# Kernel optimization log

Hardware: AMD Instinct MI355X
Metric: run time of the kernel (lower is better)

Reference implementation:

```python
import jax, jax.numpy as jnp
import numpy as np

B, S, D_IN = 128, 196, 512
H, DK, RATIO = 8, 32, 4
DV = RATIO * DK                      # 128
QKV_DIM = H * (2 * DK + DV)          # 1536
PROJ_IN = H * DV                     # 1024
EPS = 1e-3                           # keras BatchNormalization default epsilon
SCALE = DK ** (-0.5)


def hard_swish(x):
    return x * jnp.clip(x + 3.0, 0.0, 6.0) * (1.0 / 6.0)


def setup_inputs() -> dict:
    key = jax.random.key(0)
    ks = jax.random.split(key, 12)
    inp = {
        "x": jax.random.normal(ks[0], (B, S, D_IN), dtype=jnp.float32),
        "W_qkv": jax.random.normal(ks[1], (D_IN, QKV_DIM), dtype=jnp.float32) * (D_IN ** -0.5),
        "b_qkv": jnp.zeros((QKV_DIM,), dtype=jnp.float32),
        "gamma1": jnp.ones((QKV_DIM,), dtype=jnp.float32),
        "beta1": jnp.zeros((QKV_DIM,), dtype=jnp.float32),
        "mean1": jax.random.normal(ks[2], (QKV_DIM,), dtype=jnp.float32) * 0.1,
        "var1": jax.random.uniform(ks[3], (QKV_DIM,), minval=0.5, maxval=1.5, dtype=jnp.float32),
        "W_proj": jax.random.normal(ks[4], (PROJ_IN, D_IN), dtype=jnp.float32) * (PROJ_IN ** -0.5),
        "b_proj": jnp.zeros((D_IN,), dtype=jnp.float32),
        "gamma2": jnp.ones((D_IN,), dtype=jnp.float32),
        "beta2": jnp.zeros((D_IN,), dtype=jnp.float32),
        "mean2": jax.random.normal(ks[5], (D_IN,), dtype=jnp.float32) * 0.1,
        "var2": jax.random.uniform(ks[6], (D_IN,), minval=0.5, maxval=1.5, dtype=jnp.float32),
    }
    return inp


def _bn(x, gamma, beta, mean, var):
    # inference-mode BatchNorm over the last (channel) axis
    return (x - mean) * jax.lax.rsqrt(var + EPS) * gamma + beta


def reference(x, W_qkv, b_qkv, gamma1, beta1, mean1, var1,
              W_proj, b_proj, gamma2, beta2, mean2, var2):
    # QKV projection + BN
    qkv = _bn(x @ W_qkv + b_qkv, gamma1, beta1, mean1, var1)      # [B,S,1536]
    qkv = qkv.reshape(B, S, H, 2 * DK + DV)
    q, k, v = jnp.split(qkv, [DK, 2 * DK], axis=3)                # [B,S,H,*]
    q = jnp.transpose(q, (0, 2, 1, 3))                            # [B,H,S,DK]
    k = jnp.transpose(k, (0, 2, 1, 3))
    v = jnp.transpose(v, (0, 2, 1, 3))                            # [B,H,S,DV]
    attn = jax.nn.softmax(jnp.einsum("bhqd,bhkd->bhqk", q, k) * SCALE, axis=-1)
    av = jnp.einsum("bhqk,bhkd->bhqd", attn, v)                   # [B,H,S,DV]
    # faithful to original: transpose to [B,H,DV,S] then reshape to [B,S,H*DV]
    hidden = jnp.transpose(av, (0, 1, 3, 2)).reshape(B, S, PROJ_IN)
    hidden = hard_swish(hidden)
    out = _bn(hidden @ W_proj + b_proj, gamma2, beta2, mean2, var2)  # [B,S,512]
    return out
```

## Files before the change

### kernel.cpp

```cpp
#include <hip/hip_runtime.h>
#include <math.h>

namespace {

constexpr int Bb   = 128;
constexpr int Ss   = 196;
constexpr int DIN  = 512;
constexpr int Hh   = 8;
constexpr int DKc  = 32;
constexpr int DVc  = 128;
constexpr int QKVD = 1536;
constexpr int PIN  = 1024;
constexpr int Mrows = Bb * Ss;
constexpr float EPSc   = 1e-3f;
constexpr float SCALEc = 0.17677669529663687f;

typedef __bf16 bf16x8 __attribute__((ext_vector_type(8)));
typedef __bf16 bf16x4 __attribute__((ext_vector_type(4)));
typedef float  f32x4  __attribute__((ext_vector_type(4)));

constexpr int VT_STRIDE = 232;
constexpr size_t VT_QELEMS = 8192;
constexpr size_t VT_BH = 4 * VT_QELEMS;

__device__ __forceinline__ void gl_lds16(const void* g, void* l) {
    __builtin_amdgcn_global_load_lds(
        (const __attribute__((address_space(1))) void*)g,
        (__attribute__((address_space(3))) void*)l, 16, 0, 0);
}

__global__ __launch_bounds__(256)
void prep(const float* __restrict__ W1, __bf16* __restrict__ WT1o,
          const float* __restrict__ W2, __bf16* __restrict__ WT2o,
          const float* __restrict__ x, __bf16* __restrict__ xb)
{
    int id = blockIdx.x;
    if (id >= 1280) {
        const int i = (id - 1280) * 256 + threadIdx.x;
        float4 v = ((const float4*)x)[i];
        bf16x4 o = { (__bf16)v.x, (__bf16)v.y, (__bf16)v.z, (__bf16)v.w };
        ((bf16x4*)xb)[i] = o;
        return;
    }
    __shared__ float tile[32][33];
    const float* W; __bf16* WT; int K, N, bx, by;
    if (id < 768) { W = W1; WT = WT1o; K = 512;  N = 1536; bx = id % 48; by = id / 48; }
    else { id -= 768; W = W2; WT = WT2o; K = 1024; N = 512;  bx = id % 16; by = id / 16; }
    const int n0 = bx * 32, k0 = by * 32;
    const int tx = threadIdx.x & 31, ty = threadIdx.x >> 5;
#pragma unroll
    for (int i = ty; i < 32; i += 8)
        tile[i][tx] = W[(size_t)(k0 + i) * N + n0 + tx];
    __syncthreads();
#pragma unroll
    for (int i = ty; i < 32; i += 8)
        WT[(size_t)(n0 + i) * K + k0 + tx] = (__bf16)tile[tx][i];
}

__global__ __launch_bounds__(256)
void gemm1_bn_scatter(const __bf16* __restrict__ A, const __bf16* __restrict__ BT,
                      const float* __restrict__ bias, const float* __restrict__ gamma,
                      const float* __restrict__ beta, const float* __restrict__ mean,
                      const float* __restrict__ var,
                      __bf16* __restrict__ qkvO, __bf16* __restrict__ VTp)
{
    constexpr int N = QKVD, K = DIN;
    constexpr int BM = 128, BN = 128;
    __shared__ __align__(16) char sm[65536];

    const int t    = threadIdx.x;
    const int wave = t >> 6;
    const int lane = t & 63;
    const int lr   = lane & 15;
    const int q    = lane >> 4;

    constexpr int ntiles = N / BN;
    constexpr int nwg = 196 * ntiles;
    const int bid = (blockIdx.x & 7) * (nwg >> 3) + (blockIdx.x >> 3);
    const int m0 = (bid / ntiles) * BM;
    const int n0 = (bid % ntiles) * BN;
    const int wm = (wave & 1) * 64;
    const int wn = (wave >> 1) * 64;

    const __bf16* aG0 = A  + (size_t)(m0 + (t >> 2)) * K + (t & 3) * 8;
    const __bf16* aG1 = aG0 + (size_t)64 * K;
    const __bf16* bG0 = BT + (size_t)(n0 + (t >> 2)) * K + (t & 3) * 8;
    const __bf16* bG1 = bG0 + (size_t)64 * K;

    auto STAGE = [&](int k0, int cur) {
        char* lA = sm + cur * 16384 + wave * 1024;
        char* lB = sm + 32768 + cur * 16384 + wave * 1024;
        gl_lds16(aG0 + k0,      lA);
        gl_lds16(aG1 + k0,      lA + 4096);
        gl_lds16(aG0 + k0 + 32, lA + 8192);
        gl_lds16(aG1 + k0 + 32, lA + 8192 + 4096);
        gl_lds16(bG0 + k0,      lB);
        gl_lds16(bG1 + k0,      lB + 4096);
        gl_lds16(bG0 + k0 + 32, lB + 8192);
        gl_lds16(bG1 + k0 + 32, lB + 8192 + 4096);
    };

    f32x4 acc[4][4] = {};

    STAGE(0, 0);
    __syncthreads();
    int cur = 0;
    for (int k0 = 0; k0 < K; k0 += 64) {
        if (k0 + 64 < K) STAGE(k0 + 64, cur ^ 1);
        const __bf16* Abuf = (const __bf16*)(sm + cur * 16384);
        const __bf16* Bbuf = (const __bf16*)(sm + 32768 + cur * 16384);
#pragma unroll
        for (int kk = 0; kk < 2; ++kk) {
            bf16x8 aF[4], bF[4];
#pragma unroll
            for (int i = 0; i < 4; ++i)
                aF[i] = *(const bf16x8*)(Abuf + kk * 4096 + (wm + i * 16 + lr) * 32 + q * 8);
#pragma unroll
            for (int j = 0; j < 4; ++j)
                bF[j] = *(const bf16x8*)(Bbuf + kk * 4096 + (wn + j * 16 + lr) * 32 + q * 8);
#pragma unroll
            for (int i = 0; i < 4; ++i)
#pragma unroll
                for (int j = 0; j < 4; ++j)
                    acc[i][j] = __builtin_amdgcn_mfma_f32_16x16x32_bf16(
                        aF[i], bF[j], acc[i][j], 0, 0, 0);
        }
        __syncthreads();
        cur ^= 1;
    }

    const int tmod = n0 % 384;
    const int cq0  = (tmod == 0) ? 0 : (tmod == 128 ? 64 : -1);
    const int vc0  = (tmod == 0) ? 64 : 0;
    const int nv   = (tmod == 256) ? 128 : 64;
    const bool qk_wave = (tmod == 0) ? (wn == 0) : (tmod == 128 ? (wn == 64) : false);

    __bf16* qkreg = (__bf16*)sm;
    __bf16* vreg  = (__bf16*)(sm + ((nv == 128) ? 0 : 18432));
    const int vbase = (nv == 128) ? wn : 0;

#pragma unroll
    for (int j = 0; j < 4; ++j) {
        const int n = n0 + wn + j * 16 + lr;
        const float s  = gamma[n] * rsqrtf(var[n] + EPSc);
        const float tv = fmaf(bias[n] - mean[n], s, beta[n]);
        if (qk_wave) {
#pragma unroll
            for (int i = 0; i < 4; ++i) {
                const int row = wm + i * 16 + q * 4;
#pragma unroll
                for (int r = 0; r < 4; ++r)
                    qkreg[(row + r) * 72 + j * 16 + lr] = (__bf16)fmaf(acc[i][j][r], s, tv);
            }
        } else {
#pragma unroll
            for (int i = 0; i < 4; ++i) {
                bf16x4 pk = { (__bf16)fmaf(acc[i][j][0], s, tv),
                              (__bf16)fmaf(acc[i][j][1], s, tv),
                              (__bf16)fmaf(acc[i][j][2], s, tv),
                              (__bf16)fmaf(acc[i][j][3], s, tv) };
                *(bf16x4*)(vreg + (vbase + j * 16 + lr) * 136 + wm + i * 16 + q * 4) = pk;
            }
        }
    }
    __syncthreads();

    if (cq0 >= 0) {
#pragma unroll
        for (int rr = 0; rr < 4; ++rr) {
            const int row = rr * 32 + (t >> 3);
            const int l   = t & 7;
            bf16x8 vv = *(const bf16x8*)(qkreg + row * 72 + l * 8);
            *(bf16x8*)(qkvO + (size_t)(m0 + row) * N + n0 + cq0 + l * 8) = vv;
        }
    }
    const int iters = (nv * 16) / 256;
    for (int it = 0; it < iters; ++it) {
        const int a  = it * 256 + t;
        const int cl = a >> 4;
        const int r0 = (a & 15) * 8;
        const int n  = n0 + vc0 + cl;
        const int h  = n / 192;
        const int d  = n - h * 192 - 64;
        const int mr = m0 + r0;
        const int b_ = mr / 196;
        const int s0 = mr - b_ * 196;
        __bf16* dst0 = VTp + (size_t)(b_ * 8 + h) * VT_BH
                     + (size_t)(d >> 5) * VT_QELEMS + (size_t)(d & 31) * VT_STRIDE;
        bf16x8 vv = *(const bf16x8*)(vreg + cl * 136 + r0);
        if (s0 <= 188) {
            *(bf16x8*)(dst0 + s0) = vv;
        } else {
#pragma unroll
            for (int e = 0; e < 8; ++e) {
                int se = s0 + e;
                __bf16* dst = dst0;
                if (se >= 196) { se -= 196; dst += 8 * VT_BH; }
                dst[se] = vv[e];
            }
        }
    }
}

template<int N, int K>
__global__ __launch_bounds__(256)
void gemm_bn_mfma(const __bf16* __restrict__ A, const __bf16* __restrict__ BT,
                  const float* __restrict__ bias, const float* __restrict__ gamma,
                  const float* __restrict__ beta, const float* __restrict__ mean,
                  const float* __restrict__ var, float* __restrict__ C)
{
    constexpr int BM = 128, BN = 128;
    __shared__ __align__(16) char sm[65536];
    const int t    = threadIdx.x;
    const int wave = t >> 6;
    const int lane = t & 63;
    const int lr   = lane & 15;
    const int q    = lane >> 4;
    constexpr int ntiles = N / BN;
    constexpr int nwg = 196 * ntiles;
    const int bid = (blockIdx.x & 7) * (nwg >> 3) + (blockIdx.x >> 3);
    const int m0 = (bid / ntiles) * BM;
    const int n0 = (bid % ntiles) * BN;
    const int wm = (wave & 1) * 64;
    const int wn = (wave >> 1) * 64;
    const __bf16* aG0 = A  + (size_t)(m0 + (t >> 2)) * K + (t & 3) * 8;
    const __bf16* aG1 = aG0 + (size_t)64 * K;
    const __bf16* bG0 = BT + (size_t)(n0 + (t >> 2)) * K + (t & 3) * 8;
    const __bf16* bG1 = bG0 + (size_t)64 * K;

    auto STAGE = [&](int k0, int cur) {
        char* lA = sm + cur * 16384 + wave * 1024;
        char* lB = sm + 32768 + cur * 16384 + wave * 1024;
        gl_lds16(aG0 + k0,      lA);
        gl_lds16(aG1 + k0,      lA + 4096);
        gl_lds16(aG0 + k0 + 32, lA + 8192);
        gl_lds16(aG1 + k0 + 32, lA + 8192 + 4096);
        gl_lds16(bG0 + k0,      lB);
        gl_lds16(bG1 + k0,      lB + 4096);
        gl_lds16(bG0 + k0 + 32, lB + 8192);
        gl_lds16(bG1 + k0 + 32, lB + 8192 + 4096);
    };

    f32x4 acc[4][4] = {};

    STAGE(0, 0);
    __syncthreads();
    int cur = 0;
    for (int k0 = 0; k0 < K; k0 += 64) {
        if (k0 + 64 < K) STAGE(k0 + 64, cur ^ 1);
        const __bf16* Abuf = (const __bf16*)(sm + cur * 16384);
        const __bf16* Bbuf = (const __bf16*)(sm + 32768 + cur * 16384);
#pragma unroll
        for (int kk = 0; kk < 2; ++kk) {
            bf16x8 aF[4], bF[4];
#pragma unroll
            for (int i = 0; i < 4; ++i)
                aF[i] = *(const bf16x8*)(Abuf + kk * 4096 + (wm + i * 16 + lr) * 32 + q * 8);
#pragma unroll
            for (int j = 0; j < 4; ++j)
                bF[j] = *(const bf16x8*)(Bbuf + kk * 4096 + (wn + j * 16 + lr) * 32 + q * 8);
#pragma unroll
            for (int i = 0; i < 4; ++i)
#pragma unroll
                for (int j = 0; j < 4; ++j)
                    acc[i][j] = __builtin_amdgcn_mfma_f32_16x16x32_bf16(
                        aF[i], bF[j], acc[i][j], 0, 0, 0);
        }
        __syncthreads();
        cur ^= 1;
    }
#pragma unroll
    for (int j = 0; j < 4; ++j) {
        const int n = n0 + wn + j * 16 + lr;
        const float s  = gamma[n] * rsqrtf(var[n] + EPSc);
        const float tv = fmaf(bias[n] - mean[n], s, beta[n]);
#pragma unroll
        for (int i = 0; i < 4; ++i) {
            const int mrow = m0 + wm + i * 16 + q * 4;
#pragma unroll
            for (int r = 0; r < 4; ++r)
                C[(size_t)(mrow + r) * N + n] = fmaf(acc[i][j][r], s, tv);
        }
    }
}

__global__ __launch_bounds__(1024)
void attn_mfma(const __bf16* __restrict__ qkv, const __bf16* __restrict__ VTp,
               __bf16* __restrict__ hidden)
{
    __shared__ __align__(16) char smem[145920];
    __bf16* Kb = (__bf16*)smem;

    const int t = threadIdx.x;
    const int wave = t >> 6, lane = t & 63;
    const int lr = lane & 15, q = lane >> 4;
    const int bh = blockIdx.x;
    const int b = bh >> 3, h = bh & 7;
    const __bf16* qkvb = qkv + (size_t)b * 196 * QKVD + h * 192;

    const char* gV = (const char*)(VTp + (size_t)bh * VT_BH);
    char* ldsV = smem + 113152;
    gl_lds16(gV + wave * 1024 + lane * 16, ldsV + wave * 1024);

    if (t < 196 * 4) {
        const int s = t >> 2, c = t & 3;
        bf16x8 v = *(const bf16x8*)(qkvb + (size_t)s * QKVD + 32 + c * 8);
        *(bf16x8*)(Kb + s * 40 + c * 8) = v;
    }

    __syncthreads();

    const int qt = wave;
    const bool wactive = (qt <= 12);
    __bf16* Pw = (__bf16*)(smem + 16640 + (wactive ? qt : 0) * 7424);

    if (wactive) {
        int sQ = qt * 16 + lr; if (sQ > 195) sQ = 195;
        bf16x8 aQ = *(const bf16x8*)(qkv + ((size_t)b * 196 + sQ) * QKVD + h * 192 + q * 8);

        f32x4 sc[13];
#pragma unroll
        for (int nt = 0; nt < 13; ++nt) {
            bf16x8 bK = *(const bf16x8*)(Kb + (nt * 16 + lr) * 40 + q * 8);
            f32x4 z = {0.f, 0.f, 0.f, 0.f};
            sc[nt] = __builtin_amdgcn_mfma_f32_16x16x32_bf16(aQ, bK, z, 0, 0, 0);
        }
        float mrow[4] = {-1e30f, -1e30f, -1e30f, -1e30f};
#pragma unroll
        for (int nt = 0; nt < 13; ++nt) {
            const bool valid = (nt < 12) | (lr < 4);
#pragma unroll
            for (int r = 0; r < 4; ++r) {
                float x = sc[nt][r] * SCALEc;
                sc[nt][r] = x;
                if (valid) mrow[r] = fmaxf(mrow[r], x);
            }
        }
#pragma unroll
        for (int d = 1; d < 16; d <<= 1)
#pragma unroll
            for (int r = 0; r < 4; ++r)
                mrow[r] = fmaxf(mrow[r], __shfl_xor(mrow[r], d, 64));
        float l[4] = {0.f, 0.f, 0.f, 0.f};
#pragma unroll
        for (int nt = 0; nt < 13; ++nt) {
            const bool valid = (nt < 12) | (lr < 4);
#pragma unroll
            for (int r = 0; r < 4; ++r) {
                float e = valid ? __expf(sc[nt][r] - mrow[r]) : 0.f;
                sc[nt][r] = e;
                l[r] += e;
            }
        }
#pragma unroll
        for (int d = 1; d < 16; d <<= 1)
#pragma unroll
            for (int r = 0; r < 4; ++r)
                l[r] += __shfl_xor(l[r], d, 64);
        float inv[4];
#pragma unroll
        for (int r = 0; r < 4; ++r) inv[r] = 1.f / l[r];

#pragma unroll
        for (int nt = 0; nt < 13; ++nt)
#pragma unroll
            for (int r = 0; r < 4; ++r)
                Pw[(q * 4 + r) * 232 + nt * 16 + lr] = (__bf16)(sc[nt][r] * inv[r]);
        for (int idx = lane; idx < 16 * 24; idx += 64) {
            int row = idx & 15, cz = 208 + (idx >> 4);
            Pw[row * 232 + cz] = (__bf16)0.f;
        }
    }

    const int sbase = qt * 16 + q * 4;
    const bool sval = wactive && (sbase + 3 < 196);
    __bf16* hb = hidden + (size_t)b * 200704 + (size_t)h * 25088;

    for (int q4 = 0; q4 < 4; ++q4) {
        const __bf16* Vl = (const __bf16*)(ldsV + (q4 & 1) * 16384);
        if (q4 < 3)
            gl_lds16(gV + (size_t)(q4 + 1) * 16384 + wave * 1024 + lane * 16,
                     ldsV + ((q4 + 1) & 1) * 16384 + wave * 1024);
        if (wactive) {
            f32x4 o0 = {0.f, 0.f, 0.f, 0.f}, o1 = {0.f, 0.f, 0.f, 0.f};
#pragma unroll
            for (int kk = 0; kk < 7; ++kk) {
                bf16x8 aP = *(const bf16x8*)(Pw + lr * 232 + kk * 32 + q * 8);
                bf16x8 b0 = *(const bf16x8*)(Vl + lr * 232 + kk * 32 + q * 8);
                bf16x8 b1 = *(const bf16x8*)(Vl + (16 + lr) * 232 + kk * 32 + q * 8);
                o0 = __builtin_amdgcn_mfma_f32_16x16x32_bf16(aP, b0, o0, 0, 0, 0);
                o1 = __builtin_amdgcn_mfma_f32_16x16x32_bf16(aP, b1, o1, 0, 0, 0);
            }
            if (sval) {
#pragma unroll
                for (int nt2 = 0; nt2 < 2; ++nt2) {
                    f32x4 o = nt2 ? o1 : o0;
                    const int d = q4 * 32 + nt2 * 16 + lr;
                    bf16x4 pk;
#pragma unroll
                    for (int r = 0; r < 4; ++r) {
                        float x = o[r];
                        pk[r] = (__bf16)(x * fminf(fmaxf(x + 3.f, 0.f), 6.f) * (1.f / 6.f));
                    }
                    *(bf16x4*)(hb + (size_t)d * 196 + sbase) = pk;
                }
            }
        }
        if (q4 < 3) __syncthreads();
    }
}

}

extern "C" void kernel_launch(void* const* d_in, const int* in_sizes, int n_in,
                              void* d_out, int out_size, void* d_ws, size_t ws_size,
                              hipStream_t stream)
{
    const float* x    = (const float*)d_in[0];
    const float* Wqkv = (const float*)d_in[1];
    const float* bqkv = (const float*)d_in[2];
    const float* g1   = (const float*)d_in[3];
    const float* be1  = (const float*)d_in[4];
    const float* mu1  = (const float*)d_in[5];
    const float* va1  = (const float*)d_in[6];
    const float* Wp   = (const float*)d_in[7];
    const float* bp   = (const float*)d_in[8];
    const float* g2   = (const float*)d_in[9];
    const float* be2  = (const float*)d_in[10];
    const float* mu2  = (const float*)d_in[11];
    const float* va2  = (const float*)d_in[12];

    char* ws = (char*)d_ws;
    __bf16* qkv    = (__bf16*)ws;
    __bf16* VTp    = (__bf16*)(ws + 77070336);
    __bf16* hidden = (__bf16*)(ws + 144179200);
    __bf16* xb     = (__bf16*)(ws + 195559424);
    __bf16* WT1    = (__bf16*)(ws + 221249536);
    __bf16* WT2    = (__bf16*)(ws + 222822400);
    float*  out    = (float*)d_out;

    prep<<<dim3(13824), dim3(256), 0, stream>>>(Wqkv, WT1, Wp, WT2, x, xb);

    gemm1_bn_scatter<<<dim3(196 * (QKVD / 128)), dim3(256), 0, stream>>>(
        xb, WT1, bqkv, g1, be1, mu1, va1, qkv, VTp);

    attn_mfma<<<dim3(Bb * Hh), dim3(1024), 0, stream>>>(qkv, VTp, hidden);

    gemm_bn_mfma<DIN, PIN><<<dim3(196 * (DIN / 128)), dim3(256), 0, stream>>>(
        hidden, WT2, bp, g2, be2, mu2, va2, out);
}
```

Baseline: 263.0 us.

## Restructure QKV GEMM with 128x256 tiles, triple-buffered XOR-swizzled LDS pipeline

Rewrites the QKV projection GEMM to use 512-thread workgroups with 128x256 output tiles. K-tiles of 64 are loaded through a three-stage LDS ring with XOR swizzling to avoid bank conflicts, and explicit vmcnt waits let loads overlap the MFMA work. The epilogue becomes per-wave: each wave decides whether its 64-column slice is Q/K or V and stages it in its own LDS region, so no block-wide sync is needed before the stores. In exchange it uses 144KB of LDS per block and manual waitcnt/barrier scheduling, which limits occupancy and is fragile.

```diff
diff --git a/kernel.cpp b/kernel.cpp
--- a/kernel.cpp
+++ b/kernel.cpp
@@ -57,146 +57,165 @@
         WT[(size_t)(n0 + i) * K + k0 + tx] = (__bf16)tile[tx][i];
 }
 
-__global__ __launch_bounds__(256)
+__global__ __launch_bounds__(512)
 void gemm1_bn_scatter(const __bf16* __restrict__ A, const __bf16* __restrict__ BT,
                       const float* __restrict__ bias, const float* __restrict__ gamma,
                       const float* __restrict__ beta, const float* __restrict__ mean,
                       const float* __restrict__ var,
                       __bf16* __restrict__ qkvO, __bf16* __restrict__ VTp)
 {
-    constexpr int N = QKVD, K = DIN;
-    constexpr int BM = 128, BN = 128;
-    __shared__ __align__(16) char sm[65536];
+    constexpr int K = DIN;
+    __shared__ __align__(16) char sm[147456];
 
     const int t    = threadIdx.x;
-    const int wave = t >> 6;
+    const int wid  = t >> 6;
     const int lane = t & 63;
     const int lr   = lane & 15;
     const int q    = lane >> 4;
 
-    constexpr int ntiles = N / BN;
+    constexpr int ntiles = 6;
     constexpr int nwg = 196 * ntiles;
     const int bid = (blockIdx.x & 7) * (nwg >> 3) + (blockIdx.x >> 3);
-    const int m0 = (bid / ntiles) * BM;
-    const int n0 = (bid % ntiles) * BN;
-    const int wm = (wave & 1) * 64;
-    const int wn = (wave >> 1) * 64;
-
-    const __bf16* aG0 = A  + (size_t)(m0 + (t >> 2)) * K + (t & 3) * 8;
-    const __bf16* aG1 = aG0 + (size_t)64 * K;
-    const __bf16* bG0 = BT + (size_t)(n0 + (t >> 2)) * K + (t & 3) * 8;
-    const __bf16* bG1 = bG0 + (size_t)64 * K;
-
-    auto STAGE = [&](int k0, int cur) {
-        char* lA = sm + cur * 16384 + wave * 1024;
-        char* lB = sm + 32768 + cur * 16384 + wave * 1024;
-        gl_lds16(aG0 + k0,      lA);
-        gl_lds16(aG1 + k0,      lA + 4096);
-        gl_lds16(aG0 + k0 + 32, lA + 8192);
-        gl_lds16(aG1 + k0 + 32, lA + 8192 + 4096);
-        gl_lds16(bG0 + k0,      lB);
-        gl_lds16(bG1 + k0,      lB + 4096);
-        gl_lds16(bG0 + k0 + 32, lB + 8192);
-        gl_lds16(bG1 + k0 + 32, lB + 8192 + 4096);
+    const int m0 = (bid / ntiles) * 128;
+    const int n0 = (bid % ntiles) * 256;
+    const int wm  = (wid & 1) * 64;
+    const int wnL = (wid >> 1) * 64;
+
+    char* ring0 = sm;
+    char* ring1 = sm + 49152;
+    char* ring2 = sm + 98304;
+    char* rings[3] = { ring0, ring1, ring2 };
+
+    auto STAGE = [&](int kt, char* rg) {
+#pragma unroll
+        for (int e = 0; e < 2; ++e) {
+            const int c = e * 512 + t;
+            const int gsrc = (c & 7) ^ ((c >> 3) & 7);
+            gl_lds16(A + (size_t)(m0 + (c >> 3)) * K + kt * 64 + gsrc * 8,
+                     rg + c * 16);
+        }
+#pragma unroll
+        for (int e = 0; e < 4; ++e) {
+            const int c = e * 512 + t;
+            const int gsrc = (c & 7) ^ ((c >> 3) & 7);
+            gl_lds16(BT + (size_t)(n0 + (c >> 3)) * K + kt * 64 + gsrc * 8,
+                     rg + 16384 + c * 16);
+        }
     };
 
     f32x4 acc[4][4] = {};
 
-    STAGE(0, 0);
-    __syncthreads();
-    int cur = 0;
-    for (int k0 = 0; k0 < K; k0 += 64) {
-        if (k0 + 64 < K) STAGE(k0 + 64, cur ^ 1);
-        const __bf16* Abuf = (const __bf16*)(sm + cur * 16384);
-        const __bf16* Bbuf = (const __bf16*)(sm + 32768 + cur * 16384);
-#pragma unroll
-        for (int kk = 0; kk < 2; ++kk) {
-            bf16x8 aF[4], bF[4];
-#pragma unroll
-            for (int i = 0; i < 4; ++i)
-                aF[i] = *(const bf16x8*)(Abuf + kk * 4096 + (wm + i * 16 + lr) * 32 + q * 8);
-#pragma unroll
-            for (int j = 0; j < 4; ++j)
-                bF[j] = *(const bf16x8*)(Bbuf + kk * 4096 + (wn + j * 16 + lr) * 32 + q * 8);
+    STAGE(0, ring0);
+    STAGE(1, ring1);
+    asm volatile("s_waitcnt vmcnt(6)" ::: "memory");
+    __builtin_amdgcn_s_barrier();
+    __builtin_amdgcn_sched_barrier(0);
+
+#pragma unroll
+    for (int p = 0; p < 8; ++p) {
+        if (p <= 5) STAGE(p + 2, rings[(p + 2) % 3]);
+        const char* rg = rings[p % 3];
+
+        bf16x8 aF[2][4], bF[2][4];
+#pragma unroll
+        for (int kh = 0; kh < 2; ++kh) {
+#pragma unroll
+            for (int i = 0; i < 4; ++i) {
+                const int row = wm + i * 16 + lr;
+                const int off = row * 128 + (((kh * 4 + q) ^ (row & 7)) << 4);
+                aF[kh][i] = *(const bf16x8*)(rg + off);
+            }
+#pragma unroll
+            for (int j = 0; j < 4; ++j) {
+                const int row = wnL + j * 16 + lr;
+                const int off = 16384 + row * 128 + (((kh * 4 + q) ^ (row & 7)) << 4);
+                bF[kh][j] = *(const bf16x8*)(rg + off);
+            }
+        }
+        __builtin_amdgcn_s_setprio(1);
+#pragma unroll
+        for (int kh = 0; kh < 2; ++kh)
 #pragma unroll
             for (int i = 0; i < 4; ++i)
 #pragma unroll
                 for (int j = 0; j < 4; ++j)
                     acc[i][j] = __builtin_amdgcn_mfma_f32_16x16x32_bf16(
-                        aF[i], bF[j], acc[i][j], 0, 0, 0);
-        }
-        __syncthreads();
-        cur ^= 1;
-    }
-
-    const int tmod = n0 % 384;
-    const int cq0  = (tmod == 0) ? 0 : (tmod == 128 ? 64 : -1);
-    const int vc0  = (tmod == 0) ? 64 : 0;
-    const int nv   = (tmod == 256) ? 128 : 64;
-    const bool qk_wave = (tmod == 0) ? (wn == 0) : (tmod == 128 ? (wn == 64) : false);
-
-    __bf16* qkreg = (__bf16*)sm;
-    __bf16* vreg  = (__bf16*)(sm + ((nv == 128) ? 0 : 18432));
-    const int vbase = (nv == 128) ? wn : 0;
-
-#pragma unroll
-    for (int j = 0; j < 4; ++j) {
-        const int n = n0 + wn + j * 16 + lr;
-        const float s  = gamma[n] * rsqrtf(var[n] + EPSc);
-        const float tv = fmaf(bias[n] - mean[n], s, beta[n]);
-        if (qk_wave) {
-#pragma unroll
-            for (int i = 0; i < 4; ++i) {
-                const int row = wm + i * 16 + q * 4;
+                        aF[kh][i], bF[kh][j], acc[i][j], 0, 0, 0);
+        __builtin_amdgcn_s_setprio(0);
+
+        if (p <= 5)      asm volatile("s_waitcnt vmcnt(6)" ::: "memory");
+        else if (p == 6) asm volatile("s_waitcnt vmcnt(0)" ::: "memory");
+        __builtin_amdgcn_s_barrier();
+        __builtin_amdgcn_sched_barrier(0);
+    }
+
+    char* wsl = sm + wid * 16384;
+    const int g64   = (n0 >> 6) + (wid >> 1);
+    const bool isQK = (g64 % 3) == 0;
+    const int h     = g64 / 3;
+    const int nbase = n0 + (wid >> 1) * 64;
+    const int mbase = m0 + (wid & 1) * 64;
+
+    if (isQK) {
+        __bf16* qk = (__bf16*)wsl;
+#pragma unroll
+        for (int j = 0; j < 4; ++j) {
+            const int n = nbase + j * 16 + lr;
+            const float s  = gamma[n] * rsqrtf(var[n] + EPSc);
+            const float tv = fmaf(bias[n] - mean[n], s, beta[n]);
+#pragma unroll
+            for (int i = 0; i < 4; ++i)
 #pragma unroll
                 for (int r = 0; r < 4; ++r)
-                    qkreg[(row + r) * 72 + j * 16 + lr] = (__bf16)fmaf(acc[i][j][r], s, tv);
-            }
-        } else {
+                    qk[(i * 16 + q * 4 + r) * 72 + j * 16 + lr] =
+                        (__bf16)fmaf(acc[i][j][r], s, tv);
+        }
+#pragma unroll
+        for (int rr = 0; rr < 8; ++rr) {
+            const int row = rr * 8 + (lane >> 3);
+            const int g   = lane & 7;
+            bf16x8 vv = *(const bf16x8*)(qk + row * 72 + g * 8);
+            *(bf16x8*)(qkvO + (size_t)(mbase + row) * QKVD + nbase + g * 8) = vv;
+        }
+    } else {
+        __bf16* vr = (__bf16*)wsl;
+        const int d0 = nbase - h * 192 - 64;
+#pragma unroll
+        for (int j = 0; j < 4; ++j) {
+            const int n = nbase + j * 16 + lr;
+            const float s  = gamma[n] * rsqrtf(var[n] + EPSc);
+            const float tv = fmaf(bias[n] - mean[n], s, beta[n]);
 #pragma unroll
             for (int i = 0; i < 4; ++i) {
                 bf16x4 pk = { (__bf16)fmaf(acc[i][j][0], s, tv),
                               (__bf16)fmaf(acc[i][j][1], s, tv),
                               (__bf16)fmaf(acc[i][j][2], s, tv),
                               (__bf16)fmaf(acc[i][j][3], s, tv) };
-                *(bf16x4*)(vreg + (vbase + j * 16 + lr) * 136 + wm + i * 16 + q * 4) = pk;
-            }
-        }
-    }
-    __syncthreads();
-
-    if (cq0 >= 0) {
-#pragma unroll
-        for (int rr = 0; rr < 4; ++rr) {
-            const int row = rr * 32 + (t >> 3);
-            const int l   = t & 7;
-            bf16x8 vv = *(const bf16x8*)(qkreg + row * 72 + l * 8);
-            *(bf16x8*)(qkvO + (size_t)(m0 + row) * N + n0 + cq0 + l * 8) = vv;
-        }
-    }
-    const int iters = (nv * 16) / 256;
-    for (int it = 0; it < iters; ++it) {
-        const int a  = it * 256 + t;
-        const int cl = a >> 4;
-        const int r0 = (a & 15) * 8;
-        const int n  = n0 + vc0 + cl;
-        const int h  = n / 192;
-        const int d  = n - h * 192 - 64;
-        const int mr = m0 + r0;
-        const int b_ = mr / 196;
-        const int s0 = mr - b_ * 196;
-        __bf16* dst0 = VTp + (size_t)(b_ * 8 + h) * VT_BH
-                     + (size_t)(d >> 5) * VT_QELEMS + (size_t)(d & 31) * VT_STRIDE;
-        bf16x8 vv = *(const bf16x8*)(vreg + cl * 136 + r0);
-        if (s0 <= 188) {
-            *(bf16x8*)(dst0 + s0) = vv;
-        } else {
-#pragma unroll
-            for (int e = 0; e < 8; ++e) {
-                int se = s0 + e;
-                __bf16* dst = dst0;
-                if (se >= 196) { se -= 196; dst += 8 * VT_BH; }
-                dst[se] = vv[e];
+                *(bf16x4*)(vr + (j * 16 + lr) * 72 + i * 16 + q * 4) = pk;
+            }
+        }
+#pragma unroll
+        for (int rr = 0; rr < 8; ++rr) {
+            const int idx  = rr * 64 + lane;
+            const int colL = idx >> 3;
+            const int r0   = (idx & 7) * 8;
+            const int d    = d0 + colL;
+            const int mrow = mbase + r0;
+            const int b_   = mrow / 196;
+            const int s0   = mrow - b_ * 196;
+            __bf16* dst0 = VTp + (size_t)(b_ * 8 + h) * VT_BH
+                         + (size_t)(d >> 5) * VT_QELEMS + (size_t)(d & 31) * VT_STRIDE;
+            bf16x8 vv = *(const bf16x8*)(vr + colL * 72 + r0);
+            if (s0 <= 188) {
+                *(bf16x8*)(dst0 + s0) = vv;
+            } else {
+#pragma unroll
+                for (int e = 0; e < 8; ++e) {
+                    int se = s0 + e;
+                    __bf16* dst = dst0;
+                    if (se >= 196) { se -= 196; dst += 8 * VT_BH; }
+                    dst[se] = vv[e];
+                }
             }
         }
     }
@@ -441,7 +460,7 @@
 
     prep<<<dim3(13824), dim3(256), 0, stream>>>(Wqkv, WT1, Wp, WT2, x, xb);
 
-    gemm1_bn_scatter<<<dim3(196 * (QKVD / 128)), dim3(256), 0, stream>>>(
+    gemm1_bn_scatter<<<dim3(196 * 6), dim3(512), 0, stream>>>(
         xb, WT1, bqkv, g1, be1, mu1, va1, qkv, VTp);
 
     attn_mfma<<<dim3(Bb * Hh), dim3(1024), 0, stream>>>(qkv, VTp, hidden);
```

Result: no change. 263.5 us (+0.2%).
